# Optimization experiments

Hardware: AMD Instinct MI355X
Metric: run time of the kernel (lower is better)

The kernel has to match this reference:

```python
import jax, jax.numpy as jnp
import numpy as np

D = 256
H = 8
HD = D // H
LN_EPS = 1e-5


def setup_inputs() -> dict:
    key = jax.random.key(0)
    ks = jax.random.split(key, 20)
    N = 768
    s = lambda *sh: 1.0 / np.sqrt(sh[-1])
    inp = {
        "features": jax.random.normal(ks[0], (N, D), jnp.float32),
        "boxes": jax.random.uniform(ks[1], (N, 4), jnp.float32),
        # MultiheadAttention params (torch layout: [out, in])
        "in_proj_w": jax.random.normal(ks[2], (3 * D, D), jnp.float32) * s(D),
        "in_proj_b": jnp.zeros((3 * D,), jnp.float32),
        "out_proj_w": jax.random.normal(ks[3], (D, D), jnp.float32) * s(D),
        "out_proj_b": jnp.zeros((D,), jnp.float32),
        # similarity_net params
        "w1": jax.random.normal(ks[4], (256, 3 * D + 3), jnp.float32) * s(3 * D + 3),
        "b1": jnp.zeros((256,), jnp.float32),
        "ln_g": jnp.ones((256,), jnp.float32),
        "ln_b": jnp.zeros((256,), jnp.float32),
        "w2": jax.random.normal(ks[5], (128, 256), jnp.float32) * s(256),
        "b2": jnp.zeros((128,), jnp.float32),
        "w3": jax.random.normal(ks[6], (64, 128), jnp.float32) * s(128),
        "b3": jnp.zeros((64,), jnp.float32),
        "w4": jax.random.normal(ks[7], (32, 64), jnp.float32) * s(64),
        "b4": jnp.zeros((32,), jnp.float32),
        "w5": jax.random.normal(ks[8], (1, 32), jnp.float32) * s(32),
        "b5": jnp.zeros((1,), jnp.float32),
    }
    return inp


def _mha(x, in_w, in_b, out_w, out_b):
    # x: [N, D]; torch nn.MultiheadAttention self-attention (eval mode)
    N = x.shape[0]
    qkv = x @ in_w.T + in_b                      # [N, 3D]
    q, k, v = jnp.split(qkv, 3, axis=-1)
    q = q.reshape(N, H, HD).transpose(1, 0, 2)   # [H, N, HD]
    k = k.reshape(N, H, HD).transpose(1, 0, 2)
    v = v.reshape(N, H, HD).transpose(1, 0, 2)
    scores = jnp.einsum("hnd,hmd->hnm", q, k) / np.sqrt(HD)
    attn = jax.nn.softmax(scores, axis=-1)
    o = jnp.einsum("hnm,hmd->hnd", attn, v)      # [H, N, HD]
    o = o.transpose(1, 0, 2).reshape(N, D)
    return o @ out_w.T + out_b


def reference(features, boxes, in_proj_w, in_proj_b, out_proj_w, out_proj_b,
              w1, b1, ln_g, ln_b, w2, b2, w3, b3, w4, b4, w5, b5):
    N = features.shape[0]
    att = _mha(features, in_proj_w, in_proj_b, out_proj_w, out_proj_b)  # [N, D]

    fi = jnp.broadcast_to(att[:, None, :], (N, N, D))
    fj = jnp.broadcast_to(att[None, :, :], (N, N, D))
    bi = boxes[:, None, :]
    bj = boxes[None, :, :]
    x_dist = jnp.abs(bi[:, :, 0] - bj[:, :, 0])
    y_diff = bi[:, :, 1] - bj[:, :, 1]
    spatial = jnp.stack([x_dist, jnp.abs(y_diff), y_diff], axis=-1)    # [N, N, 3]
    pairs = jnp.concatenate([fi, fj, fi * fj, spatial], axis=-1)       # [N, N, 3D+3]

    h = jax.nn.relu(pairs @ w1.T + b1)
    mu = jnp.mean(h, axis=-1, keepdims=True)
    var = jnp.var(h, axis=-1, keepdims=True)
    h = (h - mu) / jnp.sqrt(var + LN_EPS) * ln_g + ln_b
    h = jax.nn.relu(h @ w2.T + b2)
    h = jax.nn.relu(h @ w3.T + b3)
    h = jax.nn.relu(h @ w4.T + b4)
    logits = (h @ w5.T + b5)[..., 0]                                   # [N, N]

    eye = jnp.eye(N, dtype=logits.dtype)
    return logits * (1.0 - eye) - 1e9 * eye
```

## Files before the change

### kernel.cpp

```cpp
#include <hip/hip_runtime.h>


typedef __attribute__((ext_vector_type(8))) __bf16 bf16x8;
typedef __attribute__((ext_vector_type(4))) float f32x4;
typedef __attribute__((ext_vector_type(8))) int i32x8;

__device__ __forceinline__ float bf2f(unsigned short u) {
    return __uint_as_float(((unsigned int)u) << 16);
}
__device__ __forceinline__ unsigned short f2bf(float f) {
    union { __bf16 b; unsigned short u; } cv;
    cv.b = (__bf16)f;
    return cv.u;
}
__device__ __forceinline__ unsigned pk2(float lo, float hi) {
    return (unsigned)f2bf(lo) | ((unsigned)f2bf(hi) << 16);
}
__device__ __forceinline__ int pk4_fp8(float a, float b, float c, float d) {
    int w = __builtin_amdgcn_cvt_pk_fp8_f32(a, b, 0, false);
    w = __builtin_amdgcn_cvt_pk_fp8_f32(c, d, w, true);
    return w;
}
__device__ __forceinline__ unsigned char f2fp8(float v) {
    return (unsigned char)(__builtin_amdgcn_cvt_pk_fp8_f32(v, 0.f, 0, false) & 0xff);
}
__device__ __forceinline__ bf16x8 load8f_bf(const float* p) {
    float4 a = *reinterpret_cast<const float4*>(p);
    float4 b = *reinterpret_cast<const float4*>(p + 4);
    union { bf16x8 v; unsigned u[4]; } cv;
    cv.u[0] = pk2(a.x, a.y); cv.u[1] = pk2(a.z, a.w);
    cv.u[2] = pk2(b.x, b.y); cv.u[3] = pk2(b.z, b.w);
    return cv.v;
}
#define SC1 0x7F7F7F7F
#define MFMA_MX(a, b, c) __builtin_amdgcn_mfma_scale_f32_16x16x128_f8f6f4( \
        (a), (b), (c), 0, 0, 0, SC1, 0, SC1)

__global__ __launch_bounds__(256) void pack_all(
    const float* __restrict__ features, const float* __restrict__ in_proj_w,
    const float* __restrict__ in_proj_b, const float* __restrict__ out_proj_w,
    const float* __restrict__ w1, const float* __restrict__ w2,
    const float* __restrict__ w3, const float* __restrict__ w4,
    const float* __restrict__ b1, const float* __restrict__ ln_g,
    const float* __restrict__ ln_b, const float* __restrict__ b2,
    const float* __restrict__ out_proj_b,
    unsigned short* __restrict__ qkvb, unsigned short* __restrict__ Vt,
    unsigned short* __restrict__ WcatB,
    unsigned char* __restrict__ w1c_mx, unsigned char* __restrict__ w1t_f8,
    unsigned char* __restrict__ w2g_mx, unsigned char* __restrict__ w3_mx,
    unsigned char* __restrict__ w4_f8,
    float* __restrict__ bias768, float* __restrict__ c1, float* __restrict__ c2)
{
    const int blk = blockIdx.x;
    if (blk < 716) {
        int t = blk * 256 + threadIdx.x;
        if (t < 65536) {
            WcatB[t] = f2bf(out_proj_w[t]);
        } else if (t < 131072) {
            int u = t - 65536;
            int e = u & 31, lane = (u >> 5) & 63, f = u >> 11;
            int mt = f & 15, ks = f >> 4;
            int o = mt * 16 + (lane & 15);
            int k = ks * 128 + ((lane >> 4) & 3) * 32 + e;
            w1c_mx[u] = f2fp8(w1[o * 771 + 512 + k]);
        } else if (t < 139264) {
            int u = t - 131072;
            int e = u & 7, lane = (u >> 3) & 63, f = u >> 9;
            int o = f * 16 + (lane & 15);
            int k = ((lane >> 4) & 3) * 8 + e;
            float v = (k < 3) ? w1[o * 771 + 768 + k] : 0.f;
            w1t_f8[u] = f2fp8(v);
        } else if (t < 172032) {
            int u = t - 139264;
            int e = u & 31, lane = (u >> 5) & 63, f = u >> 11;
            int mt = f & 7, ks = f >> 3;
            int p = mt * 16 + (lane & 15);
            int k = ks * 128 + ((lane >> 4) & 3) * 32 + e;
            w2g_mx[u] = f2fp8(w2[p * 256 + k] * ln_g[k]);
        } else if (t < 180224) {
            int u = t - 172032;
            int e = u & 31, lane = (u >> 5) & 63, f = u >> 11;
            int o = f * 16 + (lane & 15);
            int k = ((lane >> 4) & 3) * 32 + e;
            w3_mx[u] = f2fp8(w3[o * 128 + k]);
        } else if (t < 182272) {
            int u = t - 180224;
            int e = u & 7, lane = (u >> 3) & 63, f = u >> 9;
            int l15 = lane & 15, quad = lane >> 4;
            int ct = f & 1, kc = f >> 1;
            int o = ct * 16 + l15, k = kc * 32 + quad * 8 + e;
            w4_f8[u] = f2fp8(w4[o * 64 + k]);
        } else if (t < 183040) {
            int n = t - 182272;
            if (n < 256) bias768[n] = out_proj_b[n];
            else {
                int m = n - 256;
                float s = 0.f;
                for (int d = 0; d < 256; d += 4) {
                    float4 ob = *reinterpret_cast<const float4*>(&out_proj_b[d]);
                    const float* wr = (m < 256) ? &w1[m * 771 + d]
                                                : &w1[(m - 256) * 771 + 256 + d];
                    float4 w = *reinterpret_cast<const float4*>(wr);
                    s += ob.x * w.x + ob.y * w.y + ob.z * w.z + ob.w * w.w;
                }
                bias768[n] = s + ((m < 256) ? b1[m] : 0.f);
            }
        } else if (t < 183168) {
            int p = t - 183040;
            float s2 = 0.f, s1 = 0.f;
            for (int k = 0; k < 256; k += 4) {
                float4 w = *reinterpret_cast<const float4*>(&w2[p * 256 + k]);
                float4 g = *reinterpret_cast<const float4*>(&ln_g[k]);
                float4 lb = *reinterpret_cast<const float4*>(&ln_b[k]);
                s2 += g.x * w.x + g.y * w.y + g.z * w.z + g.w * w.w;
                s1 += lb.x * w.x + lb.y * w.y + lb.z * w.z + lb.w * w.w;
            }
            c2[p] = s2;
            c1[p] = s1 + b2[p];
        }
    } else if (blk < 1228) {
        const int n = blk - 716, e = threadIdx.x;
        const float* wrow = (n < 256) ? &w1[n * 771] : &w1[(n - 256) * 771 + 256];
        float acc = 0.f;
        for (int d = 0; d < 256; d += 4) {
            float4 w = *reinterpret_cast<const float4*>(&wrow[d]);
            acc += w.x * out_proj_w[(d + 0) * 256 + e];
            acc += w.y * out_proj_w[(d + 1) * 256 + e];
            acc += w.z * out_proj_w[(d + 2) * 256 + e];
            acc += w.w * out_proj_w[(d + 3) * 256 + e];
        }
        WcatB[(256 + n) * 256 + e] = f2bf(acc);
    } else {
        const int q = blk - 1228;
        const int bm = q % 12, bn = q / 12;
        const int wv = threadIdx.x >> 6, lane = threadIdx.x & 63;
        const int l15 = lane & 15, quad = lane >> 4;
        const int row0 = bm * 64 + wv * 16;
        const int col0 = bn * 64;
        f32x4 acc[4] = {};
        for (int kc = 0; kc < 8; ++kc) {
            bf16x8 a = load8f_bf(&features[(row0 + l15) * 256 + kc * 32 + quad * 8]);
#pragma unroll
            for (int ct = 0; ct < 4; ++ct) {
                bf16x8 b = load8f_bf(&in_proj_w[(col0 + ct * 16 + l15) * 256 + kc * 32 + quad * 8]);
                acc[ct] = __builtin_amdgcn_mfma_f32_16x16x32_bf16(a, b, acc[ct], 0, 0, 0);
            }
        }
#pragma unroll
        for (int ct = 0; ct < 4; ++ct)
#pragma unroll
            for (int r = 0; r < 4; ++r) {
                int row = row0 + quad * 4 + r, col = col0 + ct * 16 + l15;
                float v = acc[ct][r] + in_proj_b[col];
                if (col < 512) qkvb[row * 768 + col] = f2bf(v);
                else           Vt[(col - 512) * 768 + row] = f2bf(v);
            }
    }
}

__global__ __launch_bounds__(256) void gemm_attab(
    const unsigned short* __restrict__ A, const unsigned short* __restrict__ W,
    const float* __restrict__ bias, float* __restrict__ att,
    float* __restrict__ AB)
{
    const int wv = threadIdx.x >> 6, lane = threadIdx.x & 63;
    const int l15 = lane & 15, quad = lane >> 4;
    const int row0 = blockIdx.x * 64 + wv * 16;
    const int col0 = blockIdx.y * 64;
    f32x4 acc[4] = {};
    for (int kc = 0; kc < 8; ++kc) {
        bf16x8 a = *reinterpret_cast<const bf16x8*>(&A[(row0 + l15) * 256 + kc * 32 + quad * 8]);
#pragma unroll
        for (int ct = 0; ct < 4; ++ct) {
            bf16x8 b = *reinterpret_cast<const bf16x8*>(&W[(col0 + ct * 16 + l15) * 256 + kc * 32 + quad * 8]);
            acc[ct] = __builtin_amdgcn_mfma_f32_16x16x32_bf16(a, b, acc[ct], 0, 0, 0);
        }
    }
#pragma unroll
    for (int ct = 0; ct < 4; ++ct)
#pragma unroll
        for (int r = 0; r < 4; ++r) {
            int row = row0 + quad * 4 + r, col = col0 + ct * 16 + l15;
            float v = acc[ct][r] + bias[col];
            if (col < 256) att[row * 256 + col] = v;
            else           AB[row * 512 + (col - 256)] = v;
        }
}

#define SP 776

__global__ __launch_bounds__(256) void attn_mfma(
    const unsigned short* __restrict__ qkvb, const unsigned short* __restrict__ Vt,
    unsigned short* __restrict__ Obf)
{
    __shared__ __align__(16) unsigned short smS[32 * SP];
    __shared__ float s_inv[32];
    const int h = blockIdx.x, q0 = blockIdx.y * 32, hb = h * 32;
    const int tid = threadIdx.x, wave = tid >> 6, lane = tid & 63;
    const int l15 = lane & 15, quad = lane >> 4;

    bf16x8 af[2];
#pragma unroll
    for (int mt = 0; mt < 2; ++mt)
        af[mt] = *reinterpret_cast<const bf16x8*>(&qkvb[(q0 + mt * 16 + l15) * 768 + hb + quad * 8]);
#pragma unroll
    for (int ct = 0; ct < 12; ++ct) {
        int n0 = wave * 192 + ct * 16;
        bf16x8 b = *reinterpret_cast<const bf16x8*>(&qkvb[(n0 + l15) * 768 + 256 + hb + quad * 8]);
#pragma unroll
        for (int mt = 0; mt < 2; ++mt) {
            f32x4 c = {};
            c = __builtin_amdgcn_mfma_f32_16x16x32_bf16(af[mt], b, c, 0, 0, 0);
#pragma unroll
            for (int r = 0; r < 4; ++r)
                smS[(mt * 16 + quad * 4 + r) * SP + n0 + l15] =
                    f2bf(c[r] * 0.17677669529663689f);
        }
    }
    __syncthreads();

    {
        const int row = tid >> 3, part = tid & 7;
        unsigned short* rp = &smS[row * SP + part * 96];
        float ls = 0.f;
#pragma unroll
        for (int c8 = 0; c8 < 12; ++c8) {
            uint4 v = *reinterpret_cast<const uint4*>(&rp[c8 * 8]);
            const unsigned short* pe = reinterpret_cast<const unsigned short*>(&v);
            unsigned short o8[8];
#pragma unroll
            for (int e = 0; e < 8; ++e) {
                float ev = __expf(bf2f(pe[e]));
                ls += ev;
                o8[e] = f2bf(ev);
            }
            *reinterpret_cast<uint4*>(&rp[c8 * 8]) = *reinterpret_cast<const uint4*>(o8);
        }
        ls += __shfl_xor(ls, 1, 64);
        ls += __shfl_xor(ls, 2, 64);
        ls += __shfl_xor(ls, 4, 64);
        if (part == 0) s_inv[row] = 1.0f / ls;
    }
    __syncthreads();

    const int row0 = (wave >> 1) * 16, cg = wave & 1;
    f32x4 accp = {};
    for (int kc = 0; kc < 24; ++kc) {
        bf16x8 a = *reinterpret_cast<const bf16x8*>(&smS[(row0 + l15) * SP + kc * 32 + quad * 8]);
        bf16x8 b = *reinterpret_cast<const bf16x8*>(&Vt[(hb + cg * 16 + l15) * 768 + kc * 32 + quad * 8]);
        accp = __builtin_amdgcn_mfma_f32_16x16x32_bf16(a, b, accp, 0, 0, 0);
    }
#pragma unroll
    for (int r = 0; r < 4; ++r) {
        int rloc = row0 + quad * 4 + r;
        Obf[(q0 + rloc) * 256 + hb + cg * 16 + l15] = f2bf(accp[r] * s_inv[rloc]);
    }
}

__global__ __launch_bounds__(512, 2) void pair_mlp(
    const float* __restrict__ att, const float* __restrict__ AB,
    const unsigned char* __restrict__ w1c_mx, const unsigned char* __restrict__ w1t_f8,
    const unsigned char* __restrict__ w2g_mx, const unsigned char* __restrict__ w3_mx,
    const unsigned char* __restrict__ w4_f8,
    const float* __restrict__ boxes,
    const float* __restrict__ c1, const float* __restrict__ c2,
    const float* __restrict__ b3, const float* __restrict__ b4,
    const float* __restrict__ w5, const float* __restrict__ b5,
    float* __restrict__ out)
{
    __shared__ __align__(16) unsigned char smH[64 * 384];
    __shared__ __align__(16) unsigned char smH1[64 * 256];
    __shared__ __align__(16) unsigned char smH2[64 * 192];
    __shared__ __align__(16) unsigned char smH3[64 * 72];
    __shared__ float s_psum[64][8], s_pssq[64][8];
    __shared__ float s_mu[64], s_rs[64];
    __shared__ float s_l5[64][2];

    const int i    = blockIdx.x;
    const int j0   = blockIdx.y * 64;
    const int tid  = threadIdx.x;
    const int wave = tid >> 6;
    const int lane = tid & 63;
    const int l15  = lane & 15;
    const int quad = lane >> 4;

    {
        const int g = tid & 63;
        const int ch = g >> 2;
        float4 fi4 = *reinterpret_cast<const float4*>(&att[i * 256 + g * 4]);
#pragma unroll 4
        for (int it = 0; it < 8; ++it) {
            int r = (tid >> 6) + it * 8;
            float4 aj = *reinterpret_cast<const float4*>(&att[(j0 + r) * 256 + g * 4]);
            int cs = ch ^ (r & 15);
            *reinterpret_cast<int*>(&smH[r * 384 + cs * 16 + (g & 3) * 4]) =
                pk4_fp8(aj.x * fi4.x, aj.y * fi4.y, aj.z * fi4.z, aj.w * fi4.w);
        }
    }
    if (tid < 64) {
        int j = j0 + tid;
        float xd = fabsf(boxes[i * 4 + 0] - boxes[j * 4 + 0]);
        float yd = boxes[i * 4 + 1] - boxes[j * 4 + 1];
        unsigned char* tb = &smH[tid * 384 + 256 + (tid & 3) * 24];
        *reinterpret_cast<int*>(tb)      = pk4_fp8(xd, fabsf(yd), yd, 0.f);
        *reinterpret_cast<int*>(tb + 4)  = 0;
        *reinterpret_cast<long long*>(tb + 8)  = 0;
        *reinterpret_cast<long long*>(tb + 16) = 0;
        *reinterpret_cast<long long*>(tb + 24) = 0;
    }
    __syncthreads();

    f32x4 acc1[2][4] = {};
#pragma unroll
    for (int ks = 0; ks < 2; ++ks) {
        i32x8 a0 = *reinterpret_cast<const i32x8*>(&w1c_mx[((ks * 16 + wave * 2 + 0) * 64 + lane) * 32]);
        i32x8 a1 = *reinterpret_cast<const i32x8*>(&w1c_mx[((ks * 16 + wave * 2 + 1) * 64 + lane) * 32]);
        const int cb = ks * 8 + quad * 2;
#pragma unroll
        for (int nt = 0; nt < 4; ++nt) {
            const unsigned char* rp = &smH[(nt * 16 + l15) * 384];
            union { i32x8 v; uint4 q[2]; } b;
            b.q[0] = *reinterpret_cast<const uint4*>(rp + ((cb    ) ^ l15) * 16);
            b.q[1] = *reinterpret_cast<const uint4*>(rp + ((cb + 1) ^ l15) * 16);
            acc1[0][nt] = MFMA_MX(a0, b.v, acc1[0][nt]);
            acc1[1][nt] = MFMA_MX(a1, b.v, acc1[1][nt]);
        }
    }
    {
        long long a0 = *reinterpret_cast<const long long*>(&w1t_f8[((wave * 2 + 0) * 64 + lane) * 8]);
        long long a1 = *reinterpret_cast<const long long*>(&w1t_f8[((wave * 2 + 1) * 64 + lane) * 8]);
#pragma unroll
        for (int nt = 0; nt < 4; ++nt) {
            long long b = *reinterpret_cast<const long long*>(
                &smH[(nt * 16 + l15) * 384 + 256 + (l15 & 3) * 24 + quad * 8]);
            acc1[0][nt] = __builtin_amdgcn_mfma_f32_16x16x32_fp8_fp8(a0, b, acc1[0][nt], 0, 0, 0);
            acc1[1][nt] = __builtin_amdgcn_mfma_f32_16x16x32_fp8_fp8(a1, b, acc1[1][nt], 0, 0, 0);
        }
    }

    const int o0 = wave * 32;
    float vsum[4] = {}, vssq[4] = {};
#pragma unroll
    for (int mt = 0; mt < 2; ++mt) {
        int o = o0 + mt * 16 + quad * 4;
        float4 Ai = *reinterpret_cast<const float4*>(&AB[i * 512 + o]);
        float AiA[4] = {Ai.x, Ai.y, Ai.z, Ai.w};
#pragma unroll
        for (int nt = 0; nt < 4; ++nt) {
            int j = nt * 16 + l15;
            float4 Bj = *reinterpret_cast<const float4*>(&AB[(j0 + j) * 512 + 256 + o]);
            float BjA[4] = {Bj.x, Bj.y, Bj.z, Bj.w};
#pragma unroll
            for (int r = 0; r < 4; ++r) {
                float v = fmaxf(acc1[mt][nt][r] + AiA[r] + BjA[r], 0.f);
                acc1[mt][nt][r] = v;
                vsum[nt] += v; vssq[nt] += v * v;
            }
        }
    }
#pragma unroll
    for (int nt = 0; nt < 4; ++nt) {
        vsum[nt] += __shfl_xor(vsum[nt], 16, 64);
        vsum[nt] += __shfl_xor(vsum[nt], 32, 64);
        vssq[nt] += __shfl_xor(vssq[nt], 16, 64);
        vssq[nt] += __shfl_xor(vssq[nt], 32, 64);
    }
    if (quad == 0)
#pragma unroll
        for (int nt = 0; nt < 4; ++nt) {
            s_psum[nt * 16 + l15][wave] = vsum[nt];
            s_pssq[nt * 16 + l15][wave] = vssq[nt];
        }
#pragma unroll
    for (int mt = 0; mt < 2; ++mt) {
        const int ch = wave * 2 + mt;
#pragma unroll
        for (int nt = 0; nt < 4; ++nt) {
            int j = nt * 16 + l15;
            *reinterpret_cast<int*>(&smH1[j * 256 + (ch ^ l15) * 16 + quad * 4]) =
                pk4_fp8(acc1[mt][nt][0], acc1[mt][nt][1], acc1[mt][nt][2], acc1[mt][nt][3]);
        }
    }
    __syncthreads();
    if (wave == 0) {
        int j = lane;
        float sm = 0.f, sq = 0.f;
#pragma unroll
        for (int w = 0; w < 8; ++w) { sm += s_psum[j][w]; sq += s_pssq[j][w]; }
        sm *= (1.0f / 256.0f); sq *= (1.0f / 256.0f);
        s_mu[j] = sm;
        s_rs[j] = rsqrtf(sq - sm * sm + 1e-5f);
    }

    f32x4 acc2[4] = {};
#pragma unroll
    for (int ks = 0; ks < 2; ++ks) {
        i32x8 a = *reinterpret_cast<const i32x8*>(&w2g_mx[((ks * 8 + wave) * 64 + lane) * 32]);
        const int cb = ks * 8 + quad * 2;
#pragma unroll
        for (int nt = 0; nt < 4; ++nt) {
            const unsigned char* rp = &smH1[(nt * 16 + l15) * 256];
            union { i32x8 v; uint4 q[2]; } b;
            b.q[0] = *reinterpret_cast<const uint4*>(rp + ((cb    ) ^ l15) * 16);
            b.q[1] = *reinterpret_cast<const uint4*>(rp + ((cb + 1) ^ l15) * 16);
            acc2[nt] = MFMA_MX(a, b.v, acc2[nt]);
        }
    }
    __syncthreads();
    {
        int p = wave * 16 + quad * 4;
        float4 C1 = *reinterpret_cast<const float4*>(&c1[p]);
        float4 C2 = *reinterpret_cast<const float4*>(&c2[p]);
        float C1A[4] = {C1.x, C1.y, C1.z, C1.w};
        float C2A[4] = {C2.x, C2.y, C2.z, C2.w};
#pragma unroll
        for (int nt = 0; nt < 4; ++nt) {
            int j = nt * 16 + l15;
            float mu = s_mu[j], rs = s_rs[j];
            float vv[4];
#pragma unroll
            for (int r = 0; r < 4; ++r)
                vv[r] = fmaxf(rs * (acc2[nt][r] - mu * C2A[r]) + C1A[r], 0.f);
            *reinterpret_cast<int*>(&smH2[j * 192 + (wave ^ (l15 & 7)) * 16 + quad * 4]) =
                pk4_fp8(vv[0], vv[1], vv[2], vv[3]);
        }
    }
    __syncthreads();

    const int qt  = wave >> 1;
    const int jh2 = wave & 1;
    f32x4 acc3[2] = {};
    {
        i32x8 a = *reinterpret_cast<const i32x8*>(&w3_mx[(qt * 64 + lane) * 32]);
        const int cb = quad * 2;
#pragma unroll
        for (int ntl = 0; ntl < 2; ++ntl) {
            int j = (jh2 * 2 + ntl) * 16 + l15;
            const unsigned char* rp = &smH2[j * 192];
            union { i32x8 v; uint4 q[2]; } b;
            b.q[0] = *reinterpret_cast<const uint4*>(rp + ((cb    ) ^ (l15 & 7)) * 16);
            b.q[1] = *reinterpret_cast<const uint4*>(rp + ((cb + 1) ^ (l15 & 7)) * 16);
            acc3[ntl] = MFMA_MX(a, b.v, acc3[ntl]);
        }
    }
    {
        int q = qt * 16 + quad * 4;
        float4 B3 = *reinterpret_cast<const float4*>(&b3[q]);
        float B3A[4] = {B3.x, B3.y, B3.z, B3.w};
#pragma unroll
        for (int ntl = 0; ntl < 2; ++ntl) {
            int j = (jh2 * 2 + ntl) * 16 + l15;
            float vv[4];
#pragma unroll
            for (int r = 0; r < 4; ++r)
                vv[r] = fmaxf(acc3[ntl][r] + B3A[r], 0.f);
            *reinterpret_cast<int*>(&smH3[j * 72 + q]) = pk4_fp8(vv[0], vv[1], vv[2], vv[3]);
        }
    }
    __syncthreads();

    const int mt4 = wave & 1;
    const int jq  = wave >> 1;
    f32x4 acc4 = {};
#pragma unroll
    for (int kc = 0; kc < 2; ++kc) {
        long long a = *reinterpret_cast<const long long*>(&w4_f8[((kc * 2 + mt4) * 64 + lane) * 8]);
        int j = jq * 16 + l15;
        long long b = *reinterpret_cast<const long long*>(&smH3[j * 72 + kc * 32 + quad * 8]);
        acc4 = __builtin_amdgcn_mfma_f32_16x16x32_fp8_fp8(a, b, acc4, 0, 0, 0);
    }
    {
        int o4 = mt4 * 16 + quad * 4;
        float4 B4 = *reinterpret_cast<const float4*>(&b4[o4]);
        float4 W5 = *reinterpret_cast<const float4*>(&w5[o4]);
        float B4A[4] = {B4.x, B4.y, B4.z, B4.w};
        float W5A[4] = {W5.x, W5.y, W5.z, W5.w};
        float part = 0.f;
#pragma unroll
        for (int r = 0; r < 4; ++r)
            part += fmaxf(acc4[r] + B4A[r], 0.f) * W5A[r];
        part += __shfl_xor(part, 16, 64);
        part += __shfl_xor(part, 32, 64);
        if (quad == 0)
            s_l5[jq * 16 + l15][mt4] = part;
    }
    __syncthreads();
    if (tid < 64) {
        int j = j0 + tid;
        float v = s_l5[tid][0] + s_l5[tid][1] + b5[0];
        out[i * 768 + j] = (j == i) ? -1.0e9f : v;
    }
}

extern "C" void kernel_launch(void* const* d_in, const int* in_sizes, int n_in,
                              void* d_out, int out_size, void* d_ws, size_t ws_size,
                              hipStream_t stream)
{
    const float* features   = (const float*)d_in[0];
    const float* boxes      = (const float*)d_in[1];
    const float* in_proj_w  = (const float*)d_in[2];
    const float* in_proj_b  = (const float*)d_in[3];
    const float* out_proj_w = (const float*)d_in[4];
    const float* out_proj_b = (const float*)d_in[5];
    const float* w1  = (const float*)d_in[6];
    const float* b1  = (const float*)d_in[7];
    const float* ln_g = (const float*)d_in[8];
    const float* ln_b = (const float*)d_in[9];
    const float* w2  = (const float*)d_in[10];
    const float* b2  = (const float*)d_in[11];
    const float* w3  = (const float*)d_in[12];
    const float* b3  = (const float*)d_in[13];
    const float* w4  = (const float*)d_in[14];
    const float* b4  = (const float*)d_in[15];
    const float* w5  = (const float*)d_in[16];
    const float* b5  = (const float*)d_in[17];
    float* out = (float*)d_out;

    char* p = (char*)d_ws;
    unsigned short* qkvb  = (unsigned short*)p; p += 768 * 768 * 2;
    unsigned short* Vt    = (unsigned short*)p; p += 256 * 768 * 2;
    unsigned short* Obf   = (unsigned short*)p; p += 768 * 256 * 2;
    unsigned short* WcatB = (unsigned short*)p; p += 196608 * 2;
    float* att = (float*)p; p += 768 * 256 * 4;
    float* AB  = (float*)p; p += 768 * 512 * 4;
    unsigned char* w1c_mx = (unsigned char*)p; p += 65536;
    unsigned char* w1t_f8 = (unsigned char*)p; p += 8192;
    unsigned char* w2g_mx = (unsigned char*)p; p += 32768;
    unsigned char* w3_mx  = (unsigned char*)p; p += 8192;
    unsigned char* w4_f8  = (unsigned char*)p; p += 2048;
    float* bias768 = (float*)p; p += 768 * 4;
    float* c1v     = (float*)p; p += 128 * 4;
    float* c2v     = (float*)p; p += 128 * 4;

    pack_all<<<dim3(1372), dim3(256), 0, stream>>>(features, in_proj_w,
        in_proj_b, out_proj_w, w1, w2, w3, w4, b1, ln_g, ln_b, b2, out_proj_b,
        qkvb, Vt, WcatB, w1c_mx, w1t_f8, w2g_mx, w3_mx, w4_f8,
        bias768, c1v, c2v);
    attn_mfma<<<dim3(8, 24), dim3(256), 0, stream>>>(qkvb, Vt, Obf);
    gemm_attab<<<dim3(12, 12), dim3(256), 0, stream>>>(Obf, WcatB, bias768,
        att, AB);
    pair_mlp<<<dim3(768, 12), dim3(512), 0, stream>>>(att, AB,
        w1c_mx, w1t_f8, w2g_mx, w3_mx, w4_f8, boxes, c1v, c2v,
        b3, b4, w5, b5, out);
}
```

Before: 283.1 us.

## Fold fi into W1 product weights and loop six j-tiles per block

The pair MLP now folds the per-row feature fi into the fi*fj slice of w1, packs that as per-wave fp8 A operands once per block, and reads pre-quantized fp8 att rows for j straight from global memory. The per-pair elementwise product and its LDS staging are gone. Each block loops over six 64-column tiles instead of one, so weight setup is amortized. LDS buffers are merged and shrunk, and occupancy hints go up to 4 blocks per CU. In exchange there are new per-block prologue costs, custom MX scale factors (fi*w*16, att*8) that change the quantization error, and larger register pressure from the held A fragments.

New measurement: 543.6 us. +92.0%, slower.

```diff
diff --git a/kernel.cpp b/kernel.cpp
--- a/kernel.cpp
+++ b/kernel.cpp
@@ -35,6 +35,10 @@
 #define SC1 0x7F7F7F7F
 #define MFMA_MX(a, b, c) __builtin_amdgcn_mfma_scale_f32_16x16x128_f8f6f4( \
         (a), (b), (c), 0, 0, 0, SC1, 0, SC1)
+#define SCA 0x7B7B7B7B
+#define SCB 0x7C7C7C7C
+#define MFMA_MX_S(a, b, c) __builtin_amdgcn_mfma_scale_f32_16x16x128_f8f6f4( \
+        (a), (b), (c), 0, 0, 0, SCA, 0, SCB)
 
 __global__ __launch_bounds__(256) void pack_all(
     const float* __restrict__ features, const float* __restrict__ in_proj_w,
@@ -161,7 +165,7 @@
 __global__ __launch_bounds__(256) void gemm_attab(
     const unsigned short* __restrict__ A, const unsigned short* __restrict__ W,
     const float* __restrict__ bias, float* __restrict__ att,
-    float* __restrict__ AB)
+    float* __restrict__ AB, unsigned char* __restrict__ att_f8)
 {
     const int wv = threadIdx.x >> 6, lane = threadIdx.x & 63;
     const int l15 = lane & 15, quad = lane >> 4;
@@ -182,8 +186,12 @@
         for (int r = 0; r < 4; ++r) {
             int row = row0 + quad * 4 + r, col = col0 + ct * 16 + l15;
             float v = acc[ct][r] + bias[col];
-            if (col < 256) att[row * 256 + col] = v;
-            else           AB[row * 512 + (col - 256)] = v;
+            if (col < 256) {
+                att[row * 256 + col] = v;
+                att_f8[row * 256 + col] = f2fp8(v * 8.0f);
+            } else {
+                AB[row * 512 + (col - 256)] = v;
+            }
         }
 }
 
@@ -257,9 +265,10 @@
     }
 }
 
-__global__ __launch_bounds__(512, 2) void pair_mlp(
-    const float* __restrict__ att, const float* __restrict__ AB,
-    const unsigned char* __restrict__ w1c_mx, const unsigned char* __restrict__ w1t_f8,
+__global__ __launch_bounds__(512, 4) void pair_mlp(
+    const float* __restrict__ att, const unsigned char* __restrict__ att_f8,
+    const float* __restrict__ AB, const float* __restrict__ w1,
+    const unsigned char* __restrict__ w1t_f8,
     const unsigned char* __restrict__ w2g_mx, const unsigned char* __restrict__ w3_mx,
     const unsigned char* __restrict__ w4_f8,
     const float* __restrict__ boxes,
@@ -268,227 +277,223 @@
     const float* __restrict__ w5, const float* __restrict__ b5,
     float* __restrict__ out)
 {
-    __shared__ __align__(16) unsigned char smH[64 * 384];
-    __shared__ __align__(16) unsigned char smH1[64 * 256];
-    __shared__ __align__(16) unsigned char smH2[64 * 192];
-    __shared__ __align__(16) unsigned char smH3[64 * 72];
+    __shared__ __align__(16) unsigned char hA[16384];
+    __shared__ __align__(16) unsigned char hB[4608];
     __shared__ float s_psum[64][8], s_pssq[64][8];
     __shared__ float s_mu[64], s_rs[64];
-    __shared__ float s_l5[64][2];
 
     const int i    = blockIdx.x;
-    const int j0   = blockIdx.y * 64;
     const int tid  = threadIdx.x;
     const int wave = tid >> 6;
     const int lane = tid & 63;
     const int l15  = lane & 15;
     const int quad = lane >> 4;
 
+    const float bi0 = boxes[i * 4 + 0], bi1 = boxes[i * 4 + 1];
+    const float b5v = b5[0];
+
+    i32x8 aW[2][2];
+#pragma unroll
+    for (int ks = 0; ks < 2; ++ks)
+#pragma unroll
+        for (int m = 0; m < 2; ++m) {
+            const int o = (wave * 2 + m) * 16 + l15;
+            const float* wr = &w1[o * 771 + 512 + ks * 128 + quad * 32];
+            const float* fr = &att[i * 256 + ks * 128 + quad * 32];
+            union { i32x8 v; int w[8]; } u;
+#pragma unroll
+            for (int c = 0; c < 8; ++c) {
+                float4 wv = *reinterpret_cast<const float4*>(&wr[c * 4]);
+                float4 fv = *reinterpret_cast<const float4*>(&fr[c * 4]);
+                u.w[c] = pk4_fp8(wv.x * fv.x * 16.f, wv.y * fv.y * 16.f,
+                                 wv.z * fv.z * 16.f, wv.w * fv.w * 16.f);
+            }
+            aW[ks][m] = u.v;
+        }
+    const long long at0 = *reinterpret_cast<const long long*>(&w1t_f8[((wave * 2 + 0) * 64 + lane) * 8]);
+    const long long at1 = *reinterpret_cast<const long long*>(&w1t_f8[((wave * 2 + 1) * 64 + lane) * 8]);
+    float AiA[2][4];
+#pragma unroll
+    for (int mt = 0; mt < 2; ++mt) {
+        float4 t4 = *reinterpret_cast<const float4*>(&AB[i * 512 + wave * 32 + mt * 16 + quad * 4]);
+        AiA[mt][0] = t4.x; AiA[mt][1] = t4.y; AiA[mt][2] = t4.z; AiA[mt][3] = t4.w;
+    }
+    float C1A[4], C2A[4], B3A[4];
     {
-        const int g = tid & 63;
-        const int ch = g >> 2;
-        float4 fi4 = *reinterpret_cast<const float4*>(&att[i * 256 + g * 4]);
-#pragma unroll 4
-        for (int it = 0; it < 8; ++it) {
-            int r = (tid >> 6) + it * 8;
-            float4 aj = *reinterpret_cast<const float4*>(&att[(j0 + r) * 256 + g * 4]);
-            int cs = ch ^ (r & 15);
-            *reinterpret_cast<int*>(&smH[r * 384 + cs * 16 + (g & 3) * 4]) =
-                pk4_fp8(aj.x * fi4.x, aj.y * fi4.y, aj.z * fi4.z, aj.w * fi4.w);
-        }
-    }
-    if (tid < 64) {
-        int j = j0 + tid;
-        float xd = fabsf(boxes[i * 4 + 0] - boxes[j * 4 + 0]);
-        float yd = boxes[i * 4 + 1] - boxes[j * 4 + 1];
-        unsigned char* tb = &smH[tid * 384 + 256 + (tid & 3) * 24];
-        *reinterpret_cast<int*>(tb)      = pk4_fp8(xd, fabsf(yd), yd, 0.f);
-        *reinterpret_cast<int*>(tb + 4)  = 0;
-        *reinterpret_cast<long long*>(tb + 8)  = 0;
-        *reinterpret_cast<long long*>(tb + 16) = 0;
-        *reinterpret_cast<long long*>(tb + 24) = 0;
-    }
-    __syncthreads();
-
-    f32x4 acc1[2][4] = {};
-#pragma unroll
-    for (int ks = 0; ks < 2; ++ks) {
-        i32x8 a0 = *reinterpret_cast<const i32x8*>(&w1c_mx[((ks * 16 + wave * 2 + 0) * 64 + lane) * 32]);
-        i32x8 a1 = *reinterpret_cast<const i32x8*>(&w1c_mx[((ks * 16 + wave * 2 + 1) * 64 + lane) * 32]);
-        const int cb = ks * 8 + quad * 2;
+        float4 t1 = *reinterpret_cast<const float4*>(&c1[wave * 16 + quad * 4]);
+        float4 t2 = *reinterpret_cast<const float4*>(&c2[wave * 16 + quad * 4]);
+        float4 t3 = *reinterpret_cast<const float4*>(&b3[(wave >> 1) * 16 + quad * 4]);
+        C1A[0]=t1.x; C1A[1]=t1.y; C1A[2]=t1.z; C1A[3]=t1.w;
+        C2A[0]=t2.x; C2A[1]=t2.y; C2A[2]=t2.z; C2A[3]=t2.w;
+        B3A[0]=t3.x; B3A[1]=t3.y; B3A[2]=t3.z; B3A[3]=t3.w;
+    }
+
+    for (int t = 0; t < 6; ++t) {
+        const int j0 = blockIdx.y * 384 + t * 64;
+
+        f32x4 acc1[2][4] = {};
 #pragma unroll
         for (int nt = 0; nt < 4; ++nt) {
-            const unsigned char* rp = &smH[(nt * 16 + l15) * 384];
-            union { i32x8 v; uint4 q[2]; } b;
-            b.q[0] = *reinterpret_cast<const uint4*>(rp + ((cb    ) ^ l15) * 16);
-            b.q[1] = *reinterpret_cast<const uint4*>(rp + ((cb + 1) ^ l15) * 16);
-            acc1[0][nt] = MFMA_MX(a0, b.v, acc1[0][nt]);
-            acc1[1][nt] = MFMA_MX(a1, b.v, acc1[1][nt]);
-        }
-    }
-    {
-        long long a0 = *reinterpret_cast<const long long*>(&w1t_f8[((wave * 2 + 0) * 64 + lane) * 8]);
-        long long a1 = *reinterpret_cast<const long long*>(&w1t_f8[((wave * 2 + 1) * 64 + lane) * 8]);
+            const int j = j0 + nt * 16 + l15;
+#pragma unroll
+            for (int ks = 0; ks < 2; ++ks) {
+                i32x8 b = *reinterpret_cast<const i32x8*>(&att_f8[j * 256 + ks * 128 + quad * 32]);
+                acc1[0][nt] = MFMA_MX_S(aW[ks][0], b, acc1[0][nt]);
+                acc1[1][nt] = MFMA_MX_S(aW[ks][1], b, acc1[1][nt]);
+            }
+            long long bt;
+            {
+                float xd = fabsf(bi0 - boxes[j * 4 + 0]);
+                float yd = bi1 - boxes[j * 4 + 1];
+                int lo = pk4_fp8(xd, fabsf(yd), yd, 0.f);
+                bt = (quad == 0) ? (long long)(unsigned)lo : 0LL;
+            }
+            acc1[0][nt] = __builtin_amdgcn_mfma_f32_16x16x32_fp8_fp8(at0, bt, acc1[0][nt], 0, 0, 0);
+            acc1[1][nt] = __builtin_amdgcn_mfma_f32_16x16x32_fp8_fp8(at1, bt, acc1[1][nt], 0, 0, 0);
+        }
+
+        {
+            float vsum[4] = {}, vssq[4] = {};
+#pragma unroll
+            for (int mt = 0; mt < 2; ++mt) {
+                const int o = wave * 32 + mt * 16 + quad * 4;
+#pragma unroll
+                for (int nt = 0; nt < 4; ++nt) {
+                    int j = j0 + nt * 16 + l15;
+                    float4 Bj = *reinterpret_cast<const float4*>(&AB[j * 512 + 256 + o]);
+                    float BjA[4] = {Bj.x, Bj.y, Bj.z, Bj.w};
+#pragma unroll
+                    for (int r = 0; r < 4; ++r) {
+                        float v = fmaxf(acc1[mt][nt][r] + AiA[mt][r] + BjA[r], 0.f);
+                        acc1[mt][nt][r] = v;
+                        vsum[nt] += v; vssq[nt] += v * v;
+                    }
+                }
+            }
+#pragma unroll
+            for (int nt = 0; nt < 4; ++nt) {
+                vsum[nt] += __shfl_xor(vsum[nt], 16, 64);
+                vsum[nt] += __shfl_xor(vsum[nt], 32, 64);
+                vssq[nt] += __shfl_xor(vssq[nt], 16, 64);
+                vssq[nt] += __shfl_xor(vssq[nt], 32, 64);
+            }
+            if (quad == 0)
+#pragma unroll
+                for (int nt = 0; nt < 4; ++nt) {
+                    s_psum[nt * 16 + l15][wave] = vsum[nt];
+                    s_pssq[nt * 16 + l15][wave] = vssq[nt];
+                }
+#pragma unroll
+            for (int mt = 0; mt < 2; ++mt) {
+                const int ch = wave * 2 + mt;
+#pragma unroll
+                for (int nt = 0; nt < 4; ++nt) {
+                    int jl = nt * 16 + l15;
+                    *reinterpret_cast<int*>(&hA[jl * 256 + (ch ^ l15) * 16 + quad * 4]) =
+                        pk4_fp8(acc1[mt][nt][0], acc1[mt][nt][1], acc1[mt][nt][2], acc1[mt][nt][3]);
+                }
+            }
+        }
+        __syncthreads();
+        if (wave == 0) {
+            int jl = lane;
+            float sm = 0.f, sq = 0.f;
+#pragma unroll
+            for (int w = 0; w < 8; ++w) { sm += s_psum[jl][w]; sq += s_pssq[jl][w]; }
+            sm *= (1.0f / 256.0f); sq *= (1.0f / 256.0f);
+            s_mu[jl] = sm;
+            s_rs[jl] = rsqrtf(sq - sm * sm + 1e-5f);
+        }
+
+        f32x4 acc2[4] = {};
+#pragma unroll
+        for (int ks = 0; ks < 2; ++ks) {
+            i32x8 a = *reinterpret_cast<const i32x8*>(&w2g_mx[((ks * 8 + wave) * 64 + lane) * 32]);
+            const int cb = ks * 8 + quad * 2;
+#pragma unroll
+            for (int nt = 0; nt < 4; ++nt) {
+                const unsigned char* rp = &hA[(nt * 16 + l15) * 256];
+                union { i32x8 v; uint4 q[2]; } b;
+                b.q[0] = *reinterpret_cast<const uint4*>(rp + ((cb    ) ^ l15) * 16);
+                b.q[1] = *reinterpret_cast<const uint4*>(rp + ((cb + 1) ^ l15) * 16);
+                acc2[nt] = MFMA_MX(a, b.v, acc2[nt]);
+            }
+        }
+        __syncthreads();
 #pragma unroll
         for (int nt = 0; nt < 4; ++nt) {
-            long long b = *reinterpret_cast<const long long*>(
-                &smH[(nt * 16 + l15) * 384 + 256 + (l15 & 3) * 24 + quad * 8]);
-            acc1[0][nt] = __builtin_amdgcn_mfma_f32_16x16x32_fp8_fp8(a0, b, acc1[0][nt], 0, 0, 0);
-            acc1[1][nt] = __builtin_amdgcn_mfma_f32_16x16x32_fp8_fp8(a1, b, acc1[1][nt], 0, 0, 0);
-        }
-    }
-
-    const int o0 = wave * 32;
-    float vsum[4] = {}, vssq[4] = {};
-#pragma unroll
-    for (int mt = 0; mt < 2; ++mt) {
-        int o = o0 + mt * 16 + quad * 4;
-        float4 Ai = *reinterpret_cast<const float4*>(&AB[i * 512 + o]);
-        float AiA[4] = {Ai.x, Ai.y, Ai.z, Ai.w};
-#pragma unroll
-        for (int nt = 0; nt < 4; ++nt) {
-            int j = nt * 16 + l15;
-            float4 Bj = *reinterpret_cast<const float4*>(&AB[(j0 + j) * 512 + 256 + o]);
-            float BjA[4] = {Bj.x, Bj.y, Bj.z, Bj.w};
-#pragma unroll
-            for (int r = 0; r < 4; ++r) {
-                float v = fmaxf(acc1[mt][nt][r] + AiA[r] + BjA[r], 0.f);
-                acc1[mt][nt][r] = v;
-                vsum[nt] += v; vssq[nt] += v * v;
-            }
-        }
-    }
-#pragma unroll
-    for (int nt = 0; nt < 4; ++nt) {
-        vsum[nt] += __shfl_xor(vsum[nt], 16, 64);
-        vsum[nt] += __shfl_xor(vsum[nt], 32, 64);
-        vssq[nt] += __shfl_xor(vssq[nt], 16, 64);
-        vssq[nt] += __shfl_xor(vssq[nt], 32, 64);
-    }
-    if (quad == 0)
-#pragma unroll
-        for (int nt = 0; nt < 4; ++nt) {
-            s_psum[nt * 16 + l15][wave] = vsum[nt];
-            s_pssq[nt * 16 + l15][wave] = vssq[nt];
-        }
-#pragma unroll
-    for (int mt = 0; mt < 2; ++mt) {
-        const int ch = wave * 2 + mt;
-#pragma unroll
-        for (int nt = 0; nt < 4; ++nt) {
-            int j = nt * 16 + l15;
-            *reinterpret_cast<int*>(&smH1[j * 256 + (ch ^ l15) * 16 + quad * 4]) =
-                pk4_fp8(acc1[mt][nt][0], acc1[mt][nt][1], acc1[mt][nt][2], acc1[mt][nt][3]);
-        }
-    }
-    __syncthreads();
-    if (wave == 0) {
-        int j = lane;
-        float sm = 0.f, sq = 0.f;
-#pragma unroll
-        for (int w = 0; w < 8; ++w) { sm += s_psum[j][w]; sq += s_pssq[j][w]; }
-        sm *= (1.0f / 256.0f); sq *= (1.0f / 256.0f);
-        s_mu[j] = sm;
-        s_rs[j] = rsqrtf(sq - sm * sm + 1e-5f);
-    }
-
-    f32x4 acc2[4] = {};
-#pragma unroll
-    for (int ks = 0; ks < 2; ++ks) {
-        i32x8 a = *reinterpret_cast<const i32x8*>(&w2g_mx[((ks * 8 + wave) * 64 + lane) * 32]);
-        const int cb = ks * 8 + quad * 2;
-#pragma unroll
-        for (int nt = 0; nt < 4; ++nt) {
-            const unsigned char* rp = &smH1[(nt * 16 + l15) * 256];
-            union { i32x8 v; uint4 q[2]; } b;
-            b.q[0] = *reinterpret_cast<const uint4*>(rp + ((cb    ) ^ l15) * 16);
-            b.q[1] = *reinterpret_cast<const uint4*>(rp + ((cb + 1) ^ l15) * 16);
-            acc2[nt] = MFMA_MX(a, b.v, acc2[nt]);
-        }
-    }
-    __syncthreads();
-    {
-        int p = wave * 16 + quad * 4;
-        float4 C1 = *reinterpret_cast<const float4*>(&c1[p]);
-        float4 C2 = *reinterpret_cast<const float4*>(&c2[p]);
-        float C1A[4] = {C1.x, C1.y, C1.z, C1.w};
-        float C2A[4] = {C2.x, C2.y, C2.z, C2.w};
-#pragma unroll
-        for (int nt = 0; nt < 4; ++nt) {
-            int j = nt * 16 + l15;
-            float mu = s_mu[j], rs = s_rs[j];
+            int jl = nt * 16 + l15;
+            float mu = s_mu[jl], rsv = s_rs[jl];
             float vv[4];
 #pragma unroll
             for (int r = 0; r < 4; ++r)
-                vv[r] = fmaxf(rs * (acc2[nt][r] - mu * C2A[r]) + C1A[r], 0.f);
-            *reinterpret_cast<int*>(&smH2[j * 192 + (wave ^ (l15 & 7)) * 16 + quad * 4]) =
+                vv[r] = fmaxf(rsv * (acc2[nt][r] - mu * C2A[r]) + C1A[r], 0.f);
+            *reinterpret_cast<int*>(&hA[jl * 192 + (wave ^ (l15 & 7)) * 16 + quad * 4]) =
                 pk4_fp8(vv[0], vv[1], vv[2], vv[3]);
         }
-    }
-    __syncthreads();
-
-    const int qt  = wave >> 1;
-    const int jh2 = wave & 1;
-    f32x4 acc3[2] = {};
-    {
-        i32x8 a = *reinterpret_cast<const i32x8*>(&w3_mx[(qt * 64 + lane) * 32]);
-        const int cb = quad * 2;
-#pragma unroll
-        for (int ntl = 0; ntl < 2; ++ntl) {
-            int j = (jh2 * 2 + ntl) * 16 + l15;
-            const unsigned char* rp = &smH2[j * 192];
-            union { i32x8 v; uint4 q[2]; } b;
-            b.q[0] = *reinterpret_cast<const uint4*>(rp + ((cb    ) ^ (l15 & 7)) * 16);
-            b.q[1] = *reinterpret_cast<const uint4*>(rp + ((cb + 1) ^ (l15 & 7)) * 16);
-            acc3[ntl] = MFMA_MX(a, b.v, acc3[ntl]);
-        }
-    }
-    {
-        int q = qt * 16 + quad * 4;
-        float4 B3 = *reinterpret_cast<const float4*>(&b3[q]);
-        float B3A[4] = {B3.x, B3.y, B3.z, B3.w};
-#pragma unroll
-        for (int ntl = 0; ntl < 2; ++ntl) {
-            int j = (jh2 * 2 + ntl) * 16 + l15;
-            float vv[4];
-#pragma unroll
-            for (int r = 0; r < 4; ++r)
-                vv[r] = fmaxf(acc3[ntl][r] + B3A[r], 0.f);
-            *reinterpret_cast<int*>(&smH3[j * 72 + q]) = pk4_fp8(vv[0], vv[1], vv[2], vv[3]);
-        }
-    }
-    __syncthreads();
-
-    const int mt4 = wave & 1;
-    const int jq  = wave >> 1;
-    f32x4 acc4 = {};
-#pragma unroll
-    for (int kc = 0; kc < 2; ++kc) {
-        long long a = *reinterpret_cast<const long long*>(&w4_f8[((kc * 2 + mt4) * 64 + lane) * 8]);
-        int j = jq * 16 + l15;
-        long long b = *reinterpret_cast<const long long*>(&smH3[j * 72 + kc * 32 + quad * 8]);
-        acc4 = __builtin_amdgcn_mfma_f32_16x16x32_fp8_fp8(a, b, acc4, 0, 0, 0);
-    }
-    {
-        int o4 = mt4 * 16 + quad * 4;
-        float4 B4 = *reinterpret_cast<const float4*>(&b4[o4]);
-        float4 W5 = *reinterpret_cast<const float4*>(&w5[o4]);
-        float B4A[4] = {B4.x, B4.y, B4.z, B4.w};
-        float W5A[4] = {W5.x, W5.y, W5.z, W5.w};
-        float part = 0.f;
-#pragma unroll
-        for (int r = 0; r < 4; ++r)
-            part += fmaxf(acc4[r] + B4A[r], 0.f) * W5A[r];
-        part += __shfl_xor(part, 16, 64);
-        part += __shfl_xor(part, 32, 64);
-        if (quad == 0)
-            s_l5[jq * 16 + l15][mt4] = part;
-    }
-    __syncthreads();
-    if (tid < 64) {
-        int j = j0 + tid;
-        float v = s_l5[tid][0] + s_l5[tid][1] + b5[0];
-        out[i * 768 + j] = (j == i) ? -1.0e9f : v;
+        __syncthreads();
+
+        {
+            const int qt  = wave >> 1;
+            const int jh2 = wave & 1;
+            f32x4 acc3[2] = {};
+            i32x8 a = *reinterpret_cast<const i32x8*>(&w3_mx[(qt * 64 + lane) * 32]);
+            const int cb = quad * 2;
+#pragma unroll
+            for (int ntl = 0; ntl < 2; ++ntl) {
+                int jl = (jh2 * 2 + ntl) * 16 + l15;
+                const unsigned char* rp = &hA[jl * 192];
+                union { i32x8 v; uint4 q[2]; } b;
+                b.q[0] = *reinterpret_cast<const uint4*>(rp + ((cb    ) ^ (l15 & 7)) * 16);
+                b.q[1] = *reinterpret_cast<const uint4*>(rp + ((cb + 1) ^ (l15 & 7)) * 16);
+                acc3[ntl] = MFMA_MX(a, b.v, acc3[ntl]);
+            }
+            const int q = qt * 16 + quad * 4;
+#pragma unroll
+            for (int ntl = 0; ntl < 2; ++ntl) {
+                int jl = (jh2 * 2 + ntl) * 16 + l15;
+                float vv[4];
+#pragma unroll
+                for (int r = 0; r < 4; ++r)
+                    vv[r] = fmaxf(acc3[ntl][r] + B3A[r], 0.f);
+                *reinterpret_cast<int*>(&hB[jl * 72 + q]) = pk4_fp8(vv[0], vv[1], vv[2], vv[3]);
+            }
+        }
+        __syncthreads();
+
+        if (wave < 4) {
+            const int jq = wave;
+            f32x4 acc4[2] = {};
+#pragma unroll
+            for (int kc = 0; kc < 2; ++kc) {
+                long long b = *reinterpret_cast<const long long*>(
+                    &hB[(jq * 16 + l15) * 72 + kc * 32 + quad * 8]);
+#pragma unroll
+                for (int tt = 0; tt < 2; ++tt) {
+                    long long a = *reinterpret_cast<const long long*>(
+                        &w4_f8[((kc * 2 + tt) * 64 + lane) * 8]);
+                    acc4[tt] = __builtin_amdgcn_mfma_f32_16x16x32_fp8_fp8(a, b, acc4[tt], 0, 0, 0);
+                }
+            }
+            float part = 0.f;
+#pragma unroll
+            for (int tt = 0; tt < 2; ++tt) {
+                const int o4 = tt * 16 + quad * 4;
+                float4 B4 = *reinterpret_cast<const float4*>(&b4[o4]);
+                float4 W5 = *reinterpret_cast<const float4*>(&w5[o4]);
+                float B4A[4] = {B4.x, B4.y, B4.z, B4.w};
+                float W5A[4] = {W5.x, W5.y, W5.z, W5.w};
+#pragma unroll
+                for (int r = 0; r < 4; ++r)
+                    part += fmaxf(acc4[tt][r] + B4A[r], 0.f) * W5A[r];
+            }
+            part += __shfl_xor(part, 16, 64);
+            part += __shfl_xor(part, 32, 64);
+            if (quad == 0) {
+                int j = j0 + jq * 16 + l15;
+                out[i * 768 + j] = (j == i) ? -1.0e9f : part + b5v;
+            }
+        }
     }
 }
 
@@ -528,6 +533,7 @@
     unsigned char* w2g_mx = (unsigned char*)p; p += 32768;
     unsigned char* w3_mx  = (unsigned char*)p; p += 8192;
     unsigned char* w4_f8  = (unsigned char*)p; p += 2048;
+    unsigned char* att_f8 = (unsigned char*)p; p += 768 * 256;
     float* bias768 = (float*)p; p += 768 * 4;
     float* c1v     = (float*)p; p += 128 * 4;
     float* c2v     = (float*)p; p += 128 * 4;
@@ -538,8 +544,8 @@
         bias768, c1v, c2v);
     attn_mfma<<<dim3(8, 24), dim3(256), 0, stream>>>(qkvb, Vt, Obf);
     gemm_attab<<<dim3(12, 12), dim3(256), 0, stream>>>(Obf, WcatB, bias768,
-        att, AB);
-    pair_mlp<<<dim3(768, 12), dim3(512), 0, stream>>>(att, AB,
-        w1c_mx, w1t_f8, w2g_mx, w3_mx, w4_f8, boxes, c1v, c2v,
+        att, AB, att_f8);
+    pair_mlp<<<dim3(768, 2), dim3(512), 0, stream>>>(att, att_f8, AB, w1,
+        w1t_f8, w2g_mx, w3_mx, w4_f8, boxes, c1v, c2v,
         b3, b4, w5, b5, out);
 }
```

## Cut block barriers via LDS atomics for LayerNorm stats and single-wave final layer

Applied to the files above, without the earlier changes.

Replaces per-wave partial LayerNorm sums plus a wave-0 reduction pass with LDS atomicAdd into per-row accumulators, letting every thread compute mean and rstd inline. This drops one reduction step and one __syncthreads. The last layer now runs on four waves, each covering both output tiles, and writes results directly, which removes the s_l5 buffer and the final barrier. It also raises wave priority around the MFMA loops. The cost is LDS atomic contention and four idle waves in the tail.

After: 313.9 us. 1.11x slower.

```diff
diff --git a/kernel.cpp b/kernel.cpp
--- a/kernel.cpp
+++ b/kernel.cpp
@@ -272,9 +272,7 @@
     __shared__ __align__(16) unsigned char smH1[64 * 256];
     __shared__ __align__(16) unsigned char smH2[64 * 192];
     __shared__ __align__(16) unsigned char smH3[64 * 72];
-    __shared__ float s_psum[64][8], s_pssq[64][8];
-    __shared__ float s_mu[64], s_rs[64];
-    __shared__ float s_l5[64][2];
+    __shared__ float s_sum[64], s_ssq[64];
 
     const int i    = blockIdx.x;
     const int j0   = blockIdx.y * 64;
@@ -307,10 +305,13 @@
         *reinterpret_cast<long long*>(tb + 8)  = 0;
         *reinterpret_cast<long long*>(tb + 16) = 0;
         *reinterpret_cast<long long*>(tb + 24) = 0;
+        s_sum[tid] = 0.f;
+        s_ssq[tid] = 0.f;
     }
     __syncthreads();
 
     f32x4 acc1[2][4] = {};
+    __builtin_amdgcn_s_setprio(1);
 #pragma unroll
     for (int ks = 0; ks < 2; ++ks) {
         i32x8 a0 = *reinterpret_cast<const i32x8*>(&w1c_mx[((ks * 16 + wave * 2 + 0) * 64 + lane) * 32]);
@@ -337,6 +338,7 @@
             acc1[1][nt] = __builtin_amdgcn_mfma_f32_16x16x32_fp8_fp8(a1, b, acc1[1][nt], 0, 0, 0);
         }
     }
+    __builtin_amdgcn_s_setprio(0);
 
     const int o0 = wave * 32;
     float vsum[4] = {}, vssq[4] = {};
@@ -368,8 +370,8 @@
     if (quad == 0)
 #pragma unroll
         for (int nt = 0; nt < 4; ++nt) {
-            s_psum[nt * 16 + l15][wave] = vsum[nt];
-            s_pssq[nt * 16 + l15][wave] = vssq[nt];
+            atomicAdd(&s_sum[nt * 16 + l15], vsum[nt]);
+            atomicAdd(&s_ssq[nt * 16 + l15], vssq[nt]);
         }
 #pragma unroll
     for (int mt = 0; mt < 2; ++mt) {
@@ -382,17 +384,9 @@
         }
     }
     __syncthreads();
-    if (wave == 0) {
-        int j = lane;
-        float sm = 0.f, sq = 0.f;
-#pragma unroll
-        for (int w = 0; w < 8; ++w) { sm += s_psum[j][w]; sq += s_pssq[j][w]; }
-        sm *= (1.0f / 256.0f); sq *= (1.0f / 256.0f);
-        s_mu[j] = sm;
-        s_rs[j] = rsqrtf(sq - sm * sm + 1e-5f);
-    }
 
     f32x4 acc2[4] = {};
+    __builtin_amdgcn_s_setprio(1);
 #pragma unroll
     for (int ks = 0; ks < 2; ++ks) {
         i32x8 a = *reinterpret_cast<const i32x8*>(&w2g_mx[((ks * 8 + wave) * 64 + lane) * 32]);
@@ -406,7 +400,7 @@
             acc2[nt] = MFMA_MX(a, b.v, acc2[nt]);
         }
     }
-    __syncthreads();
+    __builtin_amdgcn_s_setprio(0);
     {
         int p = wave * 16 + quad * 4;
         float4 C1 = *reinterpret_cast<const float4*>(&c1[p]);
@@ -416,7 +410,8 @@
 #pragma unroll
         for (int nt = 0; nt < 4; ++nt) {
             int j = nt * 16 + l15;
-            float mu = s_mu[j], rs = s_rs[j];
+            float mu = s_sum[j] * (1.0f / 256.0f);
+            float rs = rsqrtf(s_ssq[j] * (1.0f / 256.0f) - mu * mu + 1e-5f);
             float vv[4];
 #pragma unroll
             for (int r = 0; r < 4; ++r)
@@ -459,36 +454,38 @@
     }
     __syncthreads();
 
-    const int mt4 = wave & 1;
-    const int jq  = wave >> 1;
-    f32x4 acc4 = {};
-#pragma unroll
-    for (int kc = 0; kc < 2; ++kc) {
-        long long a = *reinterpret_cast<const long long*>(&w4_f8[((kc * 2 + mt4) * 64 + lane) * 8]);
-        int j = jq * 16 + l15;
-        long long b = *reinterpret_cast<const long long*>(&smH3[j * 72 + kc * 32 + quad * 8]);
-        acc4 = __builtin_amdgcn_mfma_f32_16x16x32_fp8_fp8(a, b, acc4, 0, 0, 0);
-    }
-    {
-        int o4 = mt4 * 16 + quad * 4;
-        float4 B4 = *reinterpret_cast<const float4*>(&b4[o4]);
-        float4 W5 = *reinterpret_cast<const float4*>(&w5[o4]);
-        float B4A[4] = {B4.x, B4.y, B4.z, B4.w};
-        float W5A[4] = {W5.x, W5.y, W5.z, W5.w};
+    if (wave < 4) {
+        const int jq = wave;
+        f32x4 acc4[2] = {};
+#pragma unroll
+        for (int kc = 0; kc < 2; ++kc) {
+            long long b = *reinterpret_cast<const long long*>(
+                &smH3[(jq * 16 + l15) * 72 + kc * 32 + quad * 8]);
+#pragma unroll
+            for (int tt = 0; tt < 2; ++tt) {
+                long long a = *reinterpret_cast<const long long*>(
+                    &w4_f8[((kc * 2 + tt) * 64 + lane) * 8]);
+                acc4[tt] = __builtin_amdgcn_mfma_f32_16x16x32_fp8_fp8(a, b, acc4[tt], 0, 0, 0);
+            }
+        }
         float part = 0.f;
 #pragma unroll
-        for (int r = 0; r < 4; ++r)
-            part += fmaxf(acc4[r] + B4A[r], 0.f) * W5A[r];
+        for (int tt = 0; tt < 2; ++tt) {
+            const int o4 = tt * 16 + quad * 4;
+            float4 B4 = *reinterpret_cast<const float4*>(&b4[o4]);
+            float4 W5 = *reinterpret_cast<const float4*>(&w5[o4]);
+            float B4A[4] = {B4.x, B4.y, B4.z, B4.w};
+            float W5A[4] = {W5.x, W5.y, W5.z, W5.w};
+#pragma unroll
+            for (int r = 0; r < 4; ++r)
+                part += fmaxf(acc4[tt][r] + B4A[r], 0.f) * W5A[r];
+        }
         part += __shfl_xor(part, 16, 64);
         part += __shfl_xor(part, 32, 64);
-        if (quad == 0)
-            s_l5[jq * 16 + l15][mt4] = part;
-    }
-    __syncthreads();
-    if (tid < 64) {
-        int j = j0 + tid;
-        float v = s_l5[tid][0] + s_l5[tid][1] + b5[0];
-        out[i * 768 + j] = (j == i) ? -1.0e9f : v;
+        if (quad == 0) {
+            int j = j0 + jq * 16 + l15;
+            out[i * 768 + j] = (j == i) ? -1.0e9f : part + b5[0];
+        }
     }
 }
 
```
